# Kernel optimization log

Hardware: AMD Instinct MI355X
Metric: run time of the kernel (lower is better)

The kernel has to match this reference:

```python
import jax, jax.numpy as jnp
import numpy as np

B, H, S, D = 4, 16, 2048, 64
NEG_INF = -1e9  # matches torch masked_fill value of -1000000000.0


def setup_inputs() -> dict:
    key = jax.random.key(0)
    kq, kk, kv = jax.random.split(key, 3)
    query = jax.random.normal(kq, (B, H, S, D), dtype=jnp.float32)
    key_t = jax.random.normal(kk, (B, H, S, D), dtype=jnp.float32)
    value = jax.random.normal(kv, (B, H, S, D), dtype=jnp.float32)
    # causal mask, broadcast over batch and heads; 0 = masked out
    mask = jnp.tril(jnp.ones((S, S), dtype=jnp.int32))[None, None]
    return {"query": query, "key": key_t, "value": value, "mask": mask}


def reference(query, key, value, mask):
    d = query.shape[-1]
    scale = 1.0 / jnp.sqrt(jnp.float32(d))
    # [B,H,S,S] attention scores
    attn_score = jnp.einsum("bhqd,bhkd->bhqk", query, key) * scale
    masked = jnp.where(mask == 0, NEG_INF, attn_score)
    attn_prob = jax.nn.softmax(masked, axis=-1)
    out = jnp.einsum("bhqk,bhkd->bhqd", attn_prob, value)
    return out, attn_prob
```

## Files before the change

### kernel.cpp

```cpp
#include <hip/hip_runtime.h>
#include <hip/hip_bf16.h>


#define S_DIM 2048
#define D_DIM 64
#define NBH   64
#define SC2   0.18033688011112042f

typedef __attribute__((ext_vector_type(4))) float f32x4;
typedef __attribute__((ext_vector_type(8))) short bf16x8;
typedef __attribute__((ext_vector_type(4))) short bf16x4;
typedef __attribute__((ext_vector_type(4))) float floatx4;

static __device__ __forceinline__ ushort f2bf(float x) {
    __hip_bfloat16 h = __float2bfloat16(x);
    return *reinterpret_cast<ushort*>(&h);
}
static __device__ __forceinline__ bf16x8 pack8(floatx4 a, floatx4 b) {
    bf16x8 r;
    r[0]=(short)f2bf(a[0]); r[1]=(short)f2bf(a[1]); r[2]=(short)f2bf(a[2]); r[3]=(short)f2bf(a[3]);
    r[4]=(short)f2bf(b[0]); r[5]=(short)f2bf(b[1]); r[6]=(short)f2bf(b[2]); r[7]=(short)f2bf(b[3]);
    return r;
}
static __device__ __forceinline__ bf16x4 pack4f(float a, float b, float c, float d) {
    bf16x4 r;
    r[0]=(short)f2bf(a); r[1]=(short)f2bf(b); r[2]=(short)f2bf(c); r[3]=(short)f2bf(d);
    return r;
}
#define MFMA(a, b, acc) __builtin_amdgcn_mfma_f32_16x16x32_bf16((a), (b), (acc), 0, 0, 0)
#define BARLDS() asm volatile("s_waitcnt lgkmcnt(0)\n\ts_barrier" ::: "memory")
#define NT4(p, v) __builtin_nontemporal_store((v), (floatx4*)(p))

__global__ __launch_bounds__(256, 3) void attn_fwd_kernel(
    const float* __restrict__ Q, const float* __restrict__ K,
    const float* __restrict__ V, float* __restrict__ Out,
    float* __restrict__ Attn)
{
    __shared__ __align__(16) ushort KtR[2][64][72];
    __shared__ __align__(16) ushort Vt[2][64][72];
    __shared__ __align__(16) ushort Pl[4][16][40];

    const int tid = threadIdx.x;
    const int id  = blockIdx.x;

    if (id % 3 == 2) {
        const int z  = id / 3;
        const int bh = z >> 3;
        const int j  = z & 7;
        float* Attnb = Attn + (size_t)bh * (size_t)S_DIM * S_DIM;
        const floatx4 z4 = {0.f, 0.f, 0.f, 0.f};
        const int ct0 = (z % 31);
        for (int s = 0; s < 31; ++s) {
            int ct = ct0 + s; if (ct >= 31) ct -= 31;
            ct += 1;
            const int nr = ct << 3;
            float* base = Attnb + (ct << 6) + ((tid & 15) << 2);
            for (int i = (tid >> 4); i < nr; i += 16) {
                const int r = j + (i << 3);
                NT4(base + (size_t)r * S_DIM, z4);
            }
        }
        return;
    }

    const int cid  = (id / 3) * 2 + (id % 3);
    const int w    = tid >> 6;
    const int lane = tid & 63;
    const int g    = lane >> 4;
    const int c    = lane & 15;

    const int xcd  = cid & 7;
    const int slot = cid >> 3;
    const int bh   = xcd + 8 * (slot >> 4);
    const int xpr  = slot & 15;

    const float* Qb = Q + (size_t)bh * S_DIM * D_DIM;
    const float* Kb = K + (size_t)bh * S_DIM * D_DIM;
    const float* Vb = V + (size_t)bh * S_DIM * D_DIM;
    float* Outb  = Out  + (size_t)bh * S_DIM * D_DIM;
    float* Attnb = Attn + (size_t)bh * (size_t)S_DIM * S_DIM;

    const int q0L = xpr << 6;
    const int q0H = (31 - xpr) << 6;
    const int qrL = q0L + (w << 4) + c;
    const int qrH = q0H + (w << 4) + c;
    const int NTL1 = xpr + 1;
    const int NT1  = 32 - xpr;
    const int phase = cid % NT1;

    float* AttnL = Attnb + (size_t)qrL * S_DIM;
    float* AttnH = Attnb + (size_t)qrH * S_DIM;

    bf16x8 bQL0, bQL1, bQH0, bQH1;
    {
        const float* qp = Qb + (size_t)qrL * D_DIM + (g << 3);
        bQL0 = pack8(*(const floatx4*)qp,        *(const floatx4*)(qp + 4));
        bQL1 = pack8(*(const floatx4*)(qp + 32), *(const floatx4*)(qp + 36));
        qp = Qb + (size_t)qrH * D_DIM + (g << 3);
        bQH0 = pack8(*(const floatx4*)qp,        *(const floatx4*)(qp + 4));
        bQH1 = pack8(*(const floatx4*)(qp + 32), *(const floatx4*)(qp + 36));
    }

    const int kr1 = tid >> 2;
    const int kc1 = (tid & 3) << 4;
    const int vd  = tid & 63;
    const int vg16 = (tid >> 6) << 4;

    floatx4 kA, kB, kC, kD;
    {
        const float* s = Kb + ((size_t)(phase << 6) + kr1) * D_DIM + kc1;
        kA = *(const floatx4*)s;      kB = *(const floatx4*)(s + 4);
        kC = *(const floatx4*)(s + 8); kD = *(const floatx4*)(s + 12);
    }
    float laccL = 0.0f, laccH = 0.0f;

    int tq = phase;
    for (int t = 0; t < NT1; ++t) {
        ushort (*kt)[72] = KtR[t & 1];
        *(bf16x8*)&kt[kr1][kc1]     = pack8(kA, kB);
        *(bf16x8*)&kt[kr1][kc1 + 8] = pack8(kC, kD);
        BARLDS();
        const int tq1 = (tq + 1 == NT1) ? 0 : tq + 1;
        if (t + 1 < NT1) {
            const float* s = Kb + ((size_t)(tq1 << 6) + kr1) * D_DIM + kc1;
            kA = *(const floatx4*)s;       kB = *(const floatx4*)(s + 4);
            kC = *(const floatx4*)(s + 8); kD = *(const floatx4*)(s + 12);
        }
        const bool doL   = (tq < NTL1);
        const bool lastL = (tq == xpr);
        const bool lastH = (tq == NT1 - 1);
        #pragma unroll
        for (int h = 0; h < 4; ++h) {
            const bf16x8 a0 = *(const bf16x8*)&kt[(h << 4) + c][(g << 3)];
            const bf16x8 a1 = *(const bf16x8*)&kt[(h << 4) + c][(g << 3) + 32];
            f32x4 AH = {0.f, 0.f, 0.f, 0.f};
            AH = MFMA(a0, bQH0, AH);
            AH = MFMA(a1, bQH1, AH);
            #pragma unroll
            for (int r = 0; r < 4; ++r) {
                float v = AH[r] * SC2;
                if (lastH && ((tq << 6) + (h << 4) + (g << 2) + r) > qrH) v = -1e30f;
                laccH += exp2f(v);
            }
            if (doL) {
                f32x4 AL = {0.f, 0.f, 0.f, 0.f};
                AL = MFMA(a0, bQL0, AL);
                AL = MFMA(a1, bQL1, AL);
                #pragma unroll
                for (int r = 0; r < 4; ++r) {
                    float v = AL[r] * SC2;
                    if (lastL && ((tq << 6) + (h << 4) + (g << 2) + r) > qrL) v = -1e30f;
                    laccL += exp2f(v);
                }
            }
        }
        tq = tq1;
    }

    float vv[16];
    {
        const float* s = Kb + ((size_t)(phase << 6) + kr1) * D_DIM + kc1;
        kA = *(const floatx4*)s;      kB = *(const floatx4*)(s + 4);
        kC = *(const floatx4*)(s + 8); kD = *(const floatx4*)(s + 12);
        const float* sv = Vb + ((size_t)(phase << 6) + vg16) * D_DIM + vd;
        #pragma unroll
        for (int i = 0; i < 16; ++i) vv[i] = sv[(size_t)i * D_DIM];
    }

    laccL += __shfl_xor(laccL, 16);
    laccL += __shfl_xor(laccL, 32);
    laccH += __shfl_xor(laccH, 16);
    laccH += __shfl_xor(laccH, 32);
    const float linvL = 1.0f / laccL;
    const float linvH = 1.0f / laccH;

    BARLDS();

    f32x4 oL[4], oH[4];
    #pragma unroll
    for (int nb = 0; nb < 4; ++nb) {
        oL[nb] = (f32x4){0.f, 0.f, 0.f, 0.f};
        oH[nb] = (f32x4){0.f, 0.f, 0.f, 0.f};
    }

    tq = phase;
    for (int t = 0; t < NT1; ++t) {
        const int buf = t & 1;
        ushort (*kt)[72] = KtR[buf];
        *(bf16x8*)&kt[kr1][kc1]     = pack8(kA, kB);
        *(bf16x8*)&kt[kr1][kc1 + 8] = pack8(kC, kD);
        *(bf16x4*)&Vt[buf][vd][vg16]      = pack4f(vv[0],  vv[1],  vv[2],  vv[3]);
        *(bf16x4*)&Vt[buf][vd][vg16 + 4]  = pack4f(vv[4],  vv[5],  vv[6],  vv[7]);
        *(bf16x4*)&Vt[buf][vd][vg16 + 8]  = pack4f(vv[8],  vv[9],  vv[10], vv[11]);
        *(bf16x4*)&Vt[buf][vd][vg16 + 12] = pack4f(vv[12], vv[13], vv[14], vv[15]);
        BARLDS();
        const int tq1 = (tq + 1 == NT1) ? 0 : tq + 1;
        if (t + 1 < NT1) {
            const float* s = Kb + ((size_t)(tq1 << 6) + kr1) * D_DIM + kc1;
            kA = *(const floatx4*)s;       kB = *(const floatx4*)(s + 4);
            kC = *(const floatx4*)(s + 8); kD = *(const floatx4*)(s + 12);
            const float* sv = Vb + ((size_t)(tq1 << 6) + vg16) * D_DIM + vd;
            #pragma unroll
            for (int i = 0; i < 16; ++i) vv[i] = sv[(size_t)i * D_DIM];
        }
        const bool doL = (tq < NTL1);
        const bool mL  = (tq == xpr);
        const bool mH  = (tq == NT1 - 1);

        #pragma unroll
        for (int sl = 0; sl < 2; ++sl) {
            const bf16x8 vb0 = *(const bf16x8*)&Vt[buf][c     ][(sl << 5) + (g << 3)];
            const bf16x8 vb1 = *(const bf16x8*)&Vt[buf][c + 16][(sl << 5) + (g << 3)];
            const bf16x8 vb2 = *(const bf16x8*)&Vt[buf][c + 32][(sl << 5) + (g << 3)];
            const bf16x8 vb3 = *(const bf16x8*)&Vt[buf][c + 48][(sl << 5) + (g << 3)];

            #pragma unroll
            for (int h = 0; h < 2; ++h) {
                const int row = (sl << 5) + (h << 4) + c;
                const bf16x8 a0 = *(const bf16x8*)&kt[row][(g << 3)];
                const bf16x8 a1 = *(const bf16x8*)&kt[row][(g << 3) + 32];
                f32x4 AH = {0.f, 0.f, 0.f, 0.f};
                AH = MFMA(a0, bQH0, AH);
                AH = MFMA(a1, bQH1, AH);
                floatx4 pv;
                #pragma unroll
                for (int r = 0; r < 4; ++r) {
                    float v = AH[r] * SC2;
                    if (mH && ((tq << 6) + (sl << 5) + (h << 4) + (g << 2) + r) > qrH) v = -1e30f;
                    pv[r] = exp2f(v) * linvH;
                }
                NT4(AttnH + (tq << 6) + (sl << 5) + (h << 4) + (g << 2), pv);
                *(bf16x4*)&Pl[w][c][(h << 4) + (g << 2)] = pack4f(pv[0], pv[1], pv[2], pv[3]);
            }
            {
                const bf16x8 pa = *(const bf16x8*)&Pl[w][c][g << 3];
                oH[0] = MFMA(pa, vb0, oH[0]);
                oH[1] = MFMA(pa, vb1, oH[1]);
                oH[2] = MFMA(pa, vb2, oH[2]);
                oH[3] = MFMA(pa, vb3, oH[3]);
            }

            if (doL) {
                #pragma unroll
                for (int h = 0; h < 2; ++h) {
                    const int row = (sl << 5) + (h << 4) + c;
                    const bf16x8 a0 = *(const bf16x8*)&kt[row][(g << 3)];
                    const bf16x8 a1 = *(const bf16x8*)&kt[row][(g << 3) + 32];
                    f32x4 AL = {0.f, 0.f, 0.f, 0.f};
                    AL = MFMA(a0, bQL0, AL);
                    AL = MFMA(a1, bQL1, AL);
                    floatx4 pl;
                    #pragma unroll
                    for (int r = 0; r < 4; ++r) {
                        float v = AL[r] * SC2;
                        if (mL && ((tq << 6) + (sl << 5) + (h << 4) + (g << 2) + r) > qrL) v = -1e30f;
                        pl[r] = exp2f(v) * linvL;
                    }
                    NT4(AttnL + (tq << 6) + (sl << 5) + (h << 4) + (g << 2), pl);
                    *(bf16x4*)&Pl[w][c][(h << 4) + (g << 2)] = pack4f(pl[0], pl[1], pl[2], pl[3]);
                }
                const bf16x8 pa = *(const bf16x8*)&Pl[w][c][g << 3];
                oL[0] = MFMA(pa, vb0, oL[0]);
                oL[1] = MFMA(pa, vb1, oL[1]);
                oL[2] = MFMA(pa, vb2, oL[2]);
                oL[3] = MFMA(pa, vb3, oL[3]);
            }
        }
        tq = tq1;
    }

    #pragma unroll
    for (int r = 0; r < 4; ++r) {
        float* op = Outb + (size_t)(q0L + (w << 4) + (g << 2) + r) * D_DIM + c;
        __builtin_nontemporal_store(oL[0][r], op);
        __builtin_nontemporal_store(oL[1][r], op + 16);
        __builtin_nontemporal_store(oL[2][r], op + 32);
        __builtin_nontemporal_store(oL[3][r], op + 48);
        op = Outb + (size_t)(q0H + (w << 4) + (g << 2) + r) * D_DIM + c;
        __builtin_nontemporal_store(oH[0][r], op);
        __builtin_nontemporal_store(oH[1][r], op + 16);
        __builtin_nontemporal_store(oH[2][r], op + 32);
        __builtin_nontemporal_store(oH[3][r], op + 48);
    }
}

extern "C" void kernel_launch(void* const* d_in, const int* in_sizes, int n_in,
                              void* d_out, int out_size, void* d_ws, size_t ws_size,
                              hipStream_t stream) {
    const float* Q = (const float*)d_in[0];
    const float* K = (const float*)d_in[1];
    const float* V = (const float*)d_in[2];
    float* out  = (float*)d_out;
    float* attn = out + (size_t)NBH * S_DIM * D_DIM;

    attn_fwd_kernel<<<dim3(1536), 256, 0, stream>>>(Q, K, V, out, attn);
}
```

Measured before the change: 325.7 us.

## Halve grid by giving each compute block two paired query-tile jobs

```diff
diff --git a/kernel.cpp b/kernel.cpp
--- a/kernel.cpp
+++ b/kernel.cpp
@@ -44,19 +44,19 @@
     const int id  = blockIdx.x;
 
     if (id % 3 == 2) {
-        const int z  = id / 3;
-        const int bh = z >> 3;
-        const int j  = z & 7;
+        const int zid = id / 3;
+        const int bh  = zid >> 2;
+        const int j   = zid & 3;
         float* Attnb = Attn + (size_t)bh * (size_t)S_DIM * S_DIM;
         const floatx4 z4 = {0.f, 0.f, 0.f, 0.f};
-        const int ct0 = (z % 31);
+        const int ct0 = zid % 31;
         for (int s = 0; s < 31; ++s) {
             int ct = ct0 + s; if (ct >= 31) ct -= 31;
             ct += 1;
-            const int nr = ct << 3;
             float* base = Attnb + (ct << 6) + ((tid & 15) << 2);
-            for (int i = (tid >> 4); i < nr; i += 16) {
-                const int r = j + (i << 3);
+            for (int k = 0; k < ct; ++k) {
+                const int i = (tid >> 4) + (k << 4);
+                const int r = j + (i << 2);
                 NT4(base + (size_t)r * S_DIM, z4);
             }
         }
@@ -71,8 +71,8 @@
 
     const int xcd  = cid & 7;
     const int slot = cid >> 3;
-    const int bh   = xcd + 8 * (slot >> 4);
-    const int xpr  = slot & 15;
+    const int bh   = xcd + 8 * (slot >> 3);
+    const int x    = slot & 7;
 
     const float* Qb = Q + (size_t)bh * S_DIM * D_DIM;
     const float* Kb = K + (size_t)bh * S_DIM * D_DIM;
@@ -80,207 +80,213 @@
     float* Outb  = Out  + (size_t)bh * S_DIM * D_DIM;
     float* Attnb = Attn + (size_t)bh * (size_t)S_DIM * S_DIM;
 
-    const int q0L = xpr << 6;
-    const int q0H = (31 - xpr) << 6;
-    const int qrL = q0L + (w << 4) + c;
-    const int qrH = q0H + (w << 4) + c;
-    const int NTL1 = xpr + 1;
-    const int NT1  = 32 - xpr;
-    const int phase = cid % NT1;
-
-    float* AttnL = Attnb + (size_t)qrL * S_DIM;
-    float* AttnH = Attnb + (size_t)qrH * S_DIM;
-
-    bf16x8 bQL0, bQL1, bQH0, bQH1;
-    {
-        const float* qp = Qb + (size_t)qrL * D_DIM + (g << 3);
-        bQL0 = pack8(*(const floatx4*)qp,        *(const floatx4*)(qp + 4));
-        bQL1 = pack8(*(const floatx4*)(qp + 32), *(const floatx4*)(qp + 36));
-        qp = Qb + (size_t)qrH * D_DIM + (g << 3);
-        bQH0 = pack8(*(const floatx4*)qp,        *(const floatx4*)(qp + 4));
-        bQH1 = pack8(*(const floatx4*)(qp + 32), *(const floatx4*)(qp + 36));
-    }
-
     const int kr1 = tid >> 2;
     const int kc1 = (tid & 3) << 4;
     const int vd  = tid & 63;
     const int vg16 = (tid >> 6) << 4;
 
-    floatx4 kA, kB, kC, kD;
-    {
-        const float* s = Kb + ((size_t)(phase << 6) + kr1) * D_DIM + kc1;
-        kA = *(const floatx4*)s;      kB = *(const floatx4*)(s + 4);
-        kC = *(const floatx4*)(s + 8); kD = *(const floatx4*)(s + 12);
-    }
-    float laccL = 0.0f, laccH = 0.0f;
-
-    int tq = phase;
-    for (int t = 0; t < NT1; ++t) {
-        ushort (*kt)[72] = KtR[t & 1];
-        *(bf16x8*)&kt[kr1][kc1]     = pack8(kA, kB);
-        *(bf16x8*)&kt[kr1][kc1 + 8] = pack8(kC, kD);
-        BARLDS();
-        const int tq1 = (tq + 1 == NT1) ? 0 : tq + 1;
-        if (t + 1 < NT1) {
-            const float* s = Kb + ((size_t)(tq1 << 6) + kr1) * D_DIM + kc1;
-            kA = *(const floatx4*)s;       kB = *(const floatx4*)(s + 4);
+    for (int jj = 0; jj < 2; ++jj) {
+        const int aq = jj ? (16 + x) : (31 - x);
+        const int bq = jj ? (15 - x) : x;
+        const int q0L = bq << 6;
+        const int q0H = aq << 6;
+        const int NT1  = aq + 1;
+        const int NTL1 = bq + 1;
+        const int qrL = q0L + (w << 4) + c;
+        const int qrH = q0H + (w << 4) + c;
+        const int phase = cid % NT1;
+
+        float* AttnL = Attnb + (size_t)qrL * S_DIM;
+        float* AttnH = Attnb + (size_t)qrH * S_DIM;
+
+        bf16x8 bQL0, bQL1, bQH0, bQH1;
+        {
+            const float* qp = Qb + (size_t)qrL * D_DIM + (g << 3);
+            bQL0 = pack8(*(const floatx4*)qp,        *(const floatx4*)(qp + 4));
+            bQL1 = pack8(*(const floatx4*)(qp + 32), *(const floatx4*)(qp + 36));
+            qp = Qb + (size_t)qrH * D_DIM + (g << 3);
+            bQH0 = pack8(*(const floatx4*)qp,        *(const floatx4*)(qp + 4));
+            bQH1 = pack8(*(const floatx4*)(qp + 32), *(const floatx4*)(qp + 36));
+        }
+
+        floatx4 kA, kB, kC, kD;
+        {
+            const float* s = Kb + ((size_t)(phase << 6) + kr1) * D_DIM + kc1;
+            kA = *(const floatx4*)s;      kB = *(const floatx4*)(s + 4);
             kC = *(const floatx4*)(s + 8); kD = *(const floatx4*)(s + 12);
         }
-        const bool doL   = (tq < NTL1);
-        const bool lastL = (tq == xpr);
-        const bool lastH = (tq == NT1 - 1);
-        #pragma unroll
-        for (int h = 0; h < 4; ++h) {
-            const bf16x8 a0 = *(const bf16x8*)&kt[(h << 4) + c][(g << 3)];
-            const bf16x8 a1 = *(const bf16x8*)&kt[(h << 4) + c][(g << 3) + 32];
-            f32x4 AH = {0.f, 0.f, 0.f, 0.f};
-            AH = MFMA(a0, bQH0, AH);
-            AH = MFMA(a1, bQH1, AH);
+        float laccL = 0.0f, laccH = 0.0f;
+
+        int tq = phase;
+        for (int t = 0; t < NT1; ++t) {
+            ushort (*kt)[72] = KtR[t & 1];
+            *(bf16x8*)&kt[kr1][kc1]     = pack8(kA, kB);
+            *(bf16x8*)&kt[kr1][kc1 + 8] = pack8(kC, kD);
+            BARLDS();
+            const int tq1 = (tq + 1 == NT1) ? 0 : tq + 1;
+            if (t + 1 < NT1) {
+                const float* s = Kb + ((size_t)(tq1 << 6) + kr1) * D_DIM + kc1;
+                kA = *(const floatx4*)s;       kB = *(const floatx4*)(s + 4);
+                kC = *(const floatx4*)(s + 8); kD = *(const floatx4*)(s + 12);
+            }
+            const bool doL   = (tq < NTL1);
+            const bool lastL = (tq == bq);
+            const bool lastH = (tq == aq);
             #pragma unroll
-            for (int r = 0; r < 4; ++r) {
-                float v = AH[r] * SC2;
-                if (lastH && ((tq << 6) + (h << 4) + (g << 2) + r) > qrH) v = -1e30f;
-                laccH += exp2f(v);
-            }
-            if (doL) {
-                f32x4 AL = {0.f, 0.f, 0.f, 0.f};
-                AL = MFMA(a0, bQL0, AL);
-                AL = MFMA(a1, bQL1, AL);
-                #pragma unroll
-                for (int r = 0; r < 4; ++r) {
-                    float v = AL[r] * SC2;
-                    if (lastL && ((tq << 6) + (h << 4) + (g << 2) + r) > qrL) v = -1e30f;
-                    laccL += exp2f(v);
-                }
-            }
-        }
-        tq = tq1;
-    }
-
-    float vv[16];
-    {
-        const float* s = Kb + ((size_t)(phase << 6) + kr1) * D_DIM + kc1;
-        kA = *(const floatx4*)s;      kB = *(const floatx4*)(s + 4);
-        kC = *(const floatx4*)(s + 8); kD = *(const floatx4*)(s + 12);
-        const float* sv = Vb + ((size_t)(phase << 6) + vg16) * D_DIM + vd;
-        #pragma unroll
-        for (int i = 0; i < 16; ++i) vv[i] = sv[(size_t)i * D_DIM];
-    }
-
-    laccL += __shfl_xor(laccL, 16);
-    laccL += __shfl_xor(laccL, 32);
-    laccH += __shfl_xor(laccH, 16);
-    laccH += __shfl_xor(laccH, 32);
-    const float linvL = 1.0f / laccL;
-    const float linvH = 1.0f / laccH;
-
-    BARLDS();
-
-    f32x4 oL[4], oH[4];
-    #pragma unroll
-    for (int nb = 0; nb < 4; ++nb) {
-        oL[nb] = (f32x4){0.f, 0.f, 0.f, 0.f};
-        oH[nb] = (f32x4){0.f, 0.f, 0.f, 0.f};
-    }
-
-    tq = phase;
-    for (int t = 0; t < NT1; ++t) {
-        const int buf = t & 1;
-        ushort (*kt)[72] = KtR[buf];
-        *(bf16x8*)&kt[kr1][kc1]     = pack8(kA, kB);
-        *(bf16x8*)&kt[kr1][kc1 + 8] = pack8(kC, kD);
-        *(bf16x4*)&Vt[buf][vd][vg16]      = pack4f(vv[0],  vv[1],  vv[2],  vv[3]);
-        *(bf16x4*)&Vt[buf][vd][vg16 + 4]  = pack4f(vv[4],  vv[5],  vv[6],  vv[7]);
-        *(bf16x4*)&Vt[buf][vd][vg16 + 8]  = pack4f(vv[8],  vv[9],  vv[10], vv[11]);
-        *(bf16x4*)&Vt[buf][vd][vg16 + 12] = pack4f(vv[12], vv[13], vv[14], vv[15]);
-        BARLDS();
-        const int tq1 = (tq + 1 == NT1) ? 0 : tq + 1;
-        if (t + 1 < NT1) {
-            const float* s = Kb + ((size_t)(tq1 << 6) + kr1) * D_DIM + kc1;
-            kA = *(const floatx4*)s;       kB = *(const floatx4*)(s + 4);
-            kC = *(const floatx4*)(s + 8); kD = *(const floatx4*)(s + 12);
-            const float* sv = Vb + ((size_t)(tq1 << 6) + vg16) * D_DIM + vd;
-            #pragma unroll
-            for (int i = 0; i < 16; ++i) vv[i] = sv[(size_t)i * D_DIM];
-        }
-        const bool doL = (tq < NTL1);
-        const bool mL  = (tq == xpr);
-        const bool mH  = (tq == NT1 - 1);
-
-        #pragma unroll
-        for (int sl = 0; sl < 2; ++sl) {
-            const bf16x8 vb0 = *(const bf16x8*)&Vt[buf][c     ][(sl << 5) + (g << 3)];
-            const bf16x8 vb1 = *(const bf16x8*)&Vt[buf][c + 16][(sl << 5) + (g << 3)];
-            const bf16x8 vb2 = *(const bf16x8*)&Vt[buf][c + 32][(sl << 5) + (g << 3)];
-            const bf16x8 vb3 = *(const bf16x8*)&Vt[buf][c + 48][(sl << 5) + (g << 3)];
-
-            #pragma unroll
-            for (int h = 0; h < 2; ++h) {
-                const int row = (sl << 5) + (h << 4) + c;
-                const bf16x8 a0 = *(const bf16x8*)&kt[row][(g << 3)];
-                const bf16x8 a1 = *(const bf16x8*)&kt[row][(g << 3) + 32];
+            for (int h = 0; h < 4; ++h) {
+                const bf16x8 a0 = *(const bf16x8*)&kt[(h << 4) + c][(g << 3)];
+                const bf16x8 a1 = *(const bf16x8*)&kt[(h << 4) + c][(g << 3) + 32];
                 f32x4 AH = {0.f, 0.f, 0.f, 0.f};
                 AH = MFMA(a0, bQH0, AH);
                 AH = MFMA(a1, bQH1, AH);
-                floatx4 pv;
                 #pragma unroll
                 for (int r = 0; r < 4; ++r) {
                     float v = AH[r] * SC2;
-                    if (mH && ((tq << 6) + (sl << 5) + (h << 4) + (g << 2) + r) > qrH) v = -1e30f;
-                    pv[r] = exp2f(v) * linvH;
-                }
-                NT4(AttnH + (tq << 6) + (sl << 5) + (h << 4) + (g << 2), pv);
-                *(bf16x4*)&Pl[w][c][(h << 4) + (g << 2)] = pack4f(pv[0], pv[1], pv[2], pv[3]);
-            }
-            {
-                const bf16x8 pa = *(const bf16x8*)&Pl[w][c][g << 3];
-                oH[0] = MFMA(pa, vb0, oH[0]);
-                oH[1] = MFMA(pa, vb1, oH[1]);
-                oH[2] = MFMA(pa, vb2, oH[2]);
-                oH[3] = MFMA(pa, vb3, oH[3]);
-            }
-
-            if (doL) {
+                    if (lastH && ((tq << 6) + (h << 4) + (g << 2) + r) > qrH) v = -1e30f;
+                    laccH += exp2f(v);
+                }
+                if (doL) {
+                    f32x4 AL = {0.f, 0.f, 0.f, 0.f};
+                    AL = MFMA(a0, bQL0, AL);
+                    AL = MFMA(a1, bQL1, AL);
+                    #pragma unroll
+                    for (int r = 0; r < 4; ++r) {
+                        float v = AL[r] * SC2;
+                        if (lastL && ((tq << 6) + (h << 4) + (g << 2) + r) > qrL) v = -1e30f;
+                        laccL += exp2f(v);
+                    }
+                }
+            }
+            tq = tq1;
+        }
+
+        float vv[16];
+        {
+            const float* s = Kb + ((size_t)(phase << 6) + kr1) * D_DIM + kc1;
+            kA = *(const floatx4*)s;      kB = *(const floatx4*)(s + 4);
+            kC = *(const floatx4*)(s + 8); kD = *(const floatx4*)(s + 12);
+            const float* sv = Vb + ((size_t)(phase << 6) + vg16) * D_DIM + vd;
+            #pragma unroll
+            for (int i = 0; i < 16; ++i) vv[i] = sv[(size_t)i * D_DIM];
+        }
+
+        laccL += __shfl_xor(laccL, 16);
+        laccL += __shfl_xor(laccL, 32);
+        laccH += __shfl_xor(laccH, 16);
+        laccH += __shfl_xor(laccH, 32);
+        const float linvL = 1.0f / laccL;
+        const float linvH = 1.0f / laccH;
+
+        BARLDS();
+
+        f32x4 oL[4], oH[4];
+        #pragma unroll
+        for (int nb = 0; nb < 4; ++nb) {
+            oL[nb] = (f32x4){0.f, 0.f, 0.f, 0.f};
+            oH[nb] = (f32x4){0.f, 0.f, 0.f, 0.f};
+        }
+
+        tq = phase;
+        for (int t = 0; t < NT1; ++t) {
+            const int buf = t & 1;
+            ushort (*kt)[72] = KtR[buf];
+            *(bf16x8*)&kt[kr1][kc1]     = pack8(kA, kB);
+            *(bf16x8*)&kt[kr1][kc1 + 8] = pack8(kC, kD);
+            *(bf16x4*)&Vt[buf][vd][vg16]      = pack4f(vv[0],  vv[1],  vv[2],  vv[3]);
+            *(bf16x4*)&Vt[buf][vd][vg16 + 4]  = pack4f(vv[4],  vv[5],  vv[6],  vv[7]);
+            *(bf16x4*)&Vt[buf][vd][vg16 + 8]  = pack4f(vv[8],  vv[9],  vv[10], vv[11]);
+            *(bf16x4*)&Vt[buf][vd][vg16 + 12] = pack4f(vv[12], vv[13], vv[14], vv[15]);
+            BARLDS();
+            const int tq1 = (tq + 1 == NT1) ? 0 : tq + 1;
+            if (t + 1 < NT1) {
+                const float* s = Kb + ((size_t)(tq1 << 6) + kr1) * D_DIM + kc1;
+                kA = *(const floatx4*)s;       kB = *(const floatx4*)(s + 4);
+                kC = *(const floatx4*)(s + 8); kD = *(const floatx4*)(s + 12);
+                const float* sv = Vb + ((size_t)(tq1 << 6) + vg16) * D_DIM + vd;
+                #pragma unroll
+                for (int i = 0; i < 16; ++i) vv[i] = sv[(size_t)i * D_DIM];
+            }
+            const bool doL = (tq < NTL1);
+            const bool mL  = (tq == bq);
+            const bool mH  = (tq == aq);
+
+            #pragma unroll
+            for (int sl = 0; sl < 2; ++sl) {
+                const bf16x8 vb0 = *(const bf16x8*)&Vt[buf][c     ][(sl << 5) + (g << 3)];
+                const bf16x8 vb1 = *(const bf16x8*)&Vt[buf][c + 16][(sl << 5) + (g << 3)];
+                const bf16x8 vb2 = *(const bf16x8*)&Vt[buf][c + 32][(sl << 5) + (g << 3)];
+                const bf16x8 vb3 = *(const bf16x8*)&Vt[buf][c + 48][(sl << 5) + (g << 3)];
+
                 #pragma unroll
                 for (int h = 0; h < 2; ++h) {
                     const int row = (sl << 5) + (h << 4) + c;
                     const bf16x8 a0 = *(const bf16x8*)&kt[row][(g << 3)];
                     const bf16x8 a1 = *(const bf16x8*)&kt[row][(g << 3) + 32];
-                    f32x4 AL = {0.f, 0.f, 0.f, 0.f};
-                    AL = MFMA(a0, bQL0, AL);
-                    AL = MFMA(a1, bQL1, AL);
-                    floatx4 pl;
+                    f32x4 AH = {0.f, 0.f, 0.f, 0.f};
+                    AH = MFMA(a0, bQH0, AH);
+                    AH = MFMA(a1, bQH1, AH);
+                    floatx4 pv;
                     #pragma unroll
                     for (int r = 0; r < 4; ++r) {
-                        float v = AL[r] * SC2;
-                        if (mL && ((tq << 6) + (sl << 5) + (h << 4) + (g << 2) + r) > qrL) v = -1e30f;
-                        pl[r] = exp2f(v) * linvL;
+                        float v = AH[r] * SC2;
+                        if (mH && ((tq << 6) + (sl << 5) + (h << 4) + (g << 2) + r) > qrH) v = -1e30f;
+                        pv[r] = exp2f(v) * linvH;
                     }
-                    NT4(AttnL + (tq << 6) + (sl << 5) + (h << 4) + (g << 2), pl);
-                    *(bf16x4*)&Pl[w][c][(h << 4) + (g << 2)] = pack4f(pl[0], pl[1], pl[2], pl[3]);
-                }
-                const bf16x8 pa = *(const bf16x8*)&Pl[w][c][g << 3];
-                oL[0] = MFMA(pa, vb0, oL[0]);
-                oL[1] = MFMA(pa, vb1, oL[1]);
-                oL[2] = MFMA(pa, vb2, oL[2]);
-                oL[3] = MFMA(pa, vb3, oL[3]);
-            }
-        }
-        tq = tq1;
-    }
-
-    #pragma unroll
-    for (int r = 0; r < 4; ++r) {
-        float* op = Outb + (size_t)(q0L + (w << 4) + (g << 2) + r) * D_DIM + c;
-        __builtin_nontemporal_store(oL[0][r], op);
-        __builtin_nontemporal_store(oL[1][r], op + 16);
-        __builtin_nontemporal_store(oL[2][r], op + 32);
-        __builtin_nontemporal_store(oL[3][r], op + 48);
-        op = Outb + (size_t)(q0H + (w << 4) + (g << 2) + r) * D_DIM + c;
-        __builtin_nontemporal_store(oH[0][r], op);
-        __builtin_nontemporal_store(oH[1][r], op + 16);
-        __builtin_nontemporal_store(oH[2][r], op + 32);
-        __builtin_nontemporal_store(oH[3][r], op + 48);
+                    NT4(AttnH + (tq << 6) + (sl << 5) + (h << 4) + (g << 2), pv);
+                    *(bf16x4*)&Pl[w][c][(h << 4) + (g << 2)] = pack4f(pv[0], pv[1], pv[2], pv[3]);
+                }
+                {
+                    const bf16x8 pa = *(const bf16x8*)&Pl[w][c][g << 3];
+                    oH[0] = MFMA(pa, vb0, oH[0]);
+                    oH[1] = MFMA(pa, vb1, oH[1]);
+                    oH[2] = MFMA(pa, vb2, oH[2]);
+                    oH[3] = MFMA(pa, vb3, oH[3]);
+                }
+
+                if (doL) {
+                    #pragma unroll
+                    for (int h = 0; h < 2; ++h) {
+                        const int row = (sl << 5) + (h << 4) + c;
+                        const bf16x8 a0 = *(const bf16x8*)&kt[row][(g << 3)];
+                        const bf16x8 a1 = *(const bf16x8*)&kt[row][(g << 3) + 32];
+                        f32x4 AL = {0.f, 0.f, 0.f, 0.f};
+                        AL = MFMA(a0, bQL0, AL);
+                        AL = MFMA(a1, bQL1, AL);
+                        floatx4 pl;
+                        #pragma unroll
+                        for (int r = 0; r < 4; ++r) {
+                            float v = AL[r] * SC2;
+                            if (mL && ((tq << 6) + (sl << 5) + (h << 4) + (g << 2) + r) > qrL) v = -1e30f;
+                            pl[r] = exp2f(v) * linvL;
+                        }
+                        NT4(AttnL + (tq << 6) + (sl << 5) + (h << 4) + (g << 2), pl);
+                        *(bf16x4*)&Pl[w][c][(h << 4) + (g << 2)] = pack4f(pl[0], pl[1], pl[2], pl[3]);
+                    }
+                    const bf16x8 pa = *(const bf16x8*)&Pl[w][c][g << 3];
+                    oL[0] = MFMA(pa, vb0, oL[0]);
+                    oL[1] = MFMA(pa, vb1, oL[1]);
+                    oL[2] = MFMA(pa, vb2, oL[2]);
+                    oL[3] = MFMA(pa, vb3, oL[3]);
+                }
+            }
+            tq = tq1;
+        }
+
+        #pragma unroll
+        for (int r = 0; r < 4; ++r) {
+            float* op = Outb + (size_t)(q0L + (w << 4) + (g << 2) + r) * D_DIM + c;
+            __builtin_nontemporal_store(oL[0][r], op);
+            __builtin_nontemporal_store(oL[1][r], op + 16);
+            __builtin_nontemporal_store(oL[2][r], op + 32);
+            __builtin_nontemporal_store(oL[3][r], op + 48);
+            op = Outb + (size_t)(q0H + (w << 4) + (g << 2) + r) * D_DIM + c;
+            __builtin_nontemporal_store(oH[0][r], op);
+            __builtin_nontemporal_store(oH[1][r], op + 16);
+            __builtin_nontemporal_store(oH[2][r], op + 32);
+            __builtin_nontemporal_store(oH[3][r], op + 48);
+        }
+
+        BARLDS();
     }
 }
 
@@ -293,5 +299,5 @@
     float* out  = (float*)d_out;
     float* attn = out + (size_t)NBH * S_DIM * D_DIM;
 
-    attn_fwd_kernel<<<dim3(1536), 256, 0, stream>>>(Q, K, V, out, attn);
-}
+    attn_fwd_kernel<<<dim3(768), 256, 0, stream>>>(Q, K, V, out, attn);
+}
```

New measurement: 346.7 us. +6.5%, slower.
